# Performance work log

Measured on AMD Instinct MI355X. Metric: run time of the kernel, lower is better.

## Reference

```python
import jax, jax.numpy as jnp
import numpy as np

B, L_IN, D = 4, 4096, 1024
R_MIN, R_MAX = 0.9, 0.999


def setup_inputs() -> dict:
    key = jax.random.key(0)
    k0, k1, k2 = jax.random.split(key, 3)
    inputs = jax.random.normal(k0, (B, L_IN, D), jnp.float32)
    Wi = jax.random.normal(k1, (2 * D, D), jnp.float32) / np.sqrt(D)
    bi = jnp.zeros((2 * D,), jnp.float32)
    Wo = jax.random.normal(k2, (D, 2 * D), jnp.float32) / np.sqrt(2 * D)
    bo = jnp.zeros((D,), jnp.float32)
    # LRU stable-ring initialization, exactly as in the torch module
    rng = np.random.default_rng(0)
    u1 = rng.random(D)
    u2 = rng.random(D)
    v_log = np.log(-0.5 * np.log(u1 * (R_MAX ** 2 - R_MIN ** 2) + R_MIN ** 2))
    theta_log = np.log(u2 * np.pi * 2)
    gamma_log = np.log(np.sqrt(1.0 - np.exp(-np.exp(v_log)) ** 2))
    params_log = jnp.asarray(np.stack([v_log, theta_log, gamma_log]), jnp.float32)
    return {"inputs": inputs, "Wi": Wi, "bi": bi, "Wo": Wo, "bo": bo,
            "params_log": params_log}


def _lru_forward(inputs, Wi, bi, Wo, bo, params_log):
    b, l_in, d = inputs.shape
    u = inputs @ Wi.T + bi                      # [B, L, 2D]
    v, theta, gamma = jnp.exp(params_log)       # each [D]
    # torch.view_as_complex: interleaved (real, imag) pairs along last dim
    uc = u.reshape(b, l_in, d, 2)
    x = jax.lax.complex(uc[..., 0], uc[..., 1])  # [B, L, D] complex64
    log2_L = int(np.ceil(np.log2(l_in)))
    L = 2 ** log2_L
    x = jnp.pad(x, ((0, 0), (0, L - l_in), (0, 0)))
    # Blelloch-style log-depth scan: x_t = lambda * x_{t-1} + u_t,
    # lambda = exp(-v + i*theta)
    for i in range(1, log2_L + 1):
        blk = 2 ** i
        xb = x.reshape(b * L // blk, blk, d)
        x1, x2 = xb[:, : blk // 2], xb[:, blk // 2:]
        pos = jnp.arange(1, blk // 2 + 1, dtype=jnp.float32)  # [blk/2]
        lambs = jnp.exp(jax.lax.complex(-pos[:, None] * v,
                                        pos[:, None] * theta))  # [blk/2, D]
        x2 = x2 + lambs * x1[:, -1:]
        x = jnp.concatenate([x1, x2], axis=1).reshape(b, L, d)
    x = x[:, :l_in] * gamma.astype(x.dtype)     # normalize, drop padding
    xr = jnp.concatenate([x.real, x.imag], axis=-1)  # [B, L, 2D]
    out = xr @ Wo.T + bo
    return jax.nn.relu(out)


def reference(inputs, Wi, bi, Wo, bo, params_log):
    return _lru_forward(inputs, Wi, bi, Wo, bo, params_log)
```

## Files before the change

### kernel.cpp

```cpp
#include <hip/hip_runtime.h>

#define BB 4
#define LL 4096
#define DD 1024
#define SS 64
#define TT 64

typedef __attribute__((ext_vector_type(4))) float  floatx4;
typedef __attribute__((ext_vector_type(8))) short  shortx8;

static __device__ __forceinline__ unsigned short f2bf(float f) {
    unsigned int u = __float_as_uint(f);
    u += 0x7fffu + ((u >> 16) & 1u);
    return (unsigned short)(u >> 16);
}
static __device__ __forceinline__ float bf2f(unsigned short h) {
    return __uint_as_float(((unsigned int)h) << 16);
}

#define NIN4 (BB * LL * DD / 4)
#define NW4  (2 * DD * DD / 4)
__global__ void cast_all_kernel(const float4* __restrict__ s_in, ushort4* __restrict__ d_inb,
                                const float4* __restrict__ s_wi, ushort4* __restrict__ d_wib,
                                const float4* __restrict__ s_wo, ushort4* __restrict__ d_wob) {
    int i = blockIdx.x * blockDim.x + threadIdx.x;
    const float4* s; ushort4* d; int j;
    if (i < NIN4)                 { s = s_in; d = d_inb; j = i; }
    else if (i < NIN4 + NW4)      { s = s_wi; d = d_wib; j = i - NIN4; }
    else                          { s = s_wo; d = d_wob; j = i - NIN4 - NW4; }
    float4 v = s[j];
    ushort4 o;
    o.x = f2bf(v.x); o.y = f2bf(v.y); o.z = f2bf(v.z); o.w = f2bf(v.w);
    d[j] = o;
}

template<int K, int NT, int EPI>
__global__ __launch_bounds__(256)
void gemm_bt(const unsigned short* __restrict__ A,
             const unsigned short* __restrict__ B,
             const float* __restrict__ bias,
             void* __restrict__ Cp) {
    constexpr int N = NT * 128;
    __shared__ __align__(16) short As[128 * 64];
    __shared__ __align__(16) short Bs[128 * 64];

    const int tid = threadIdx.x;
    const int b   = blockIdx.x;
    const int xcd = b & 7;
    const int i2  = b >> 3;
    const int tileM = ((i2 / NT) * 8 + xcd) * 128;
    const int tileN = (i2 % NT) * 128;

    const int lane  = tid & 63;
    const int wave  = tid >> 6;
    const int wm    = (wave >> 1) * 64;
    const int wn    = (wave & 1) * 64;
    const int r16   = lane & 15;
    const int quad  = lane >> 4;

    floatx4 acc[4][4] = {};

    int rowS[4], colS[4];
#pragma unroll
    for (int n = 0; n < 4; ++n) {
        const int q = tid + n * 256;
        rowS[n] = q >> 3;
        colS[n] = ((q & 7) ^ (rowS[n] & 7)) * 8;
    }
    const int ldsBase = (tid & ~63) * 8;

    const int fx = r16 & 7;

    for (int k0 = 0; k0 < K; k0 += 64) {
#pragma unroll
        for (int n = 0; n < 4; ++n) {
            __builtin_amdgcn_global_load_lds(
                (const __attribute__((address_space(1))) void*)&A[(size_t)(tileM + rowS[n]) * K + k0 + colS[n]],
                (__attribute__((address_space(3))) void*)&As[ldsBase + n * 2048], 16, 0, 0);
            __builtin_amdgcn_global_load_lds(
                (const __attribute__((address_space(1))) void*)&B[(size_t)(tileN + rowS[n]) * K + k0 + colS[n]],
                (__attribute__((address_space(3))) void*)&Bs[ldsBase + n * 2048], 16, 0, 0);
        }
        __syncthreads();

#pragma unroll
        for (int kk = 0; kk < 2; ++kk) {
            const int slot = ((kk * 4 + quad) ^ fx) * 8;
            shortx8 af[4], bfv[4];
#pragma unroll
            for (int i = 0; i < 4; ++i)
                af[i] = *(const shortx8*)(&As[(wm + i * 16 + r16) * 64 + slot]);
#pragma unroll
            for (int j = 0; j < 4; ++j)
                bfv[j] = *(const shortx8*)(&Bs[(wn + j * 16 + r16) * 64 + slot]);
#pragma unroll
            for (int i = 0; i < 4; ++i)
#pragma unroll
                for (int j = 0; j < 4; ++j)
                    acc[i][j] = __builtin_amdgcn_mfma_f32_16x16x32_bf16(
                        af[i], bfv[j], acc[i][j], 0, 0, 0);
        }
        __syncthreads();
    }

#pragma unroll
    for (int i = 0; i < 4; ++i) {
#pragma unroll
        for (int j = 0; j < 4; ++j) {
            const int col = tileN + wn + j * 16 + r16;
            const float bv = bias[col];
#pragma unroll
            for (int r = 0; r < 4; ++r) {
                const int row = tileM + wm + i * 16 + quad * 4 + r;
                float v = acc[i][j][r] + bv;
                if (EPI == 0) {
                    ((unsigned short*)Cp)[(size_t)row * N + col] = f2bf(v);
                } else {
                    ((float*)Cp)[(size_t)row * N + col] = fmaxf(v, 0.0f);
                }
            }
        }
    }
}

__global__ __launch_bounds__(256)
void scanA(const unsigned short* __restrict__ u,
           const float* __restrict__ plog,
           float2* __restrict__ Eend) {
    const int d0 = (blockIdx.x * 256 + threadIdx.x) * 2;
    const int c = blockIdx.y, b = blockIdx.z;
    const float v0  = expf(plog[d0]),      v1  = expf(plog[d0 + 1]);
    const float th0 = expf(plog[DD + d0]), th1 = expf(plog[DD + d0 + 1]);
    const float a0 = expf(-v0), a1 = expf(-v1);
    const float lr0 = a0 * cosf(th0), li0 = a0 * sinf(th0);
    const float lr1 = a1 * cosf(th1), li1 = a1 * sinf(th1);
    float zr0 = 0.f, zi0 = 0.f, zr1 = 0.f, zi1 = 0.f;
    const unsigned short* up = u + (size_t)(b * LL + c * TT) * (2 * DD) + 2 * d0;
#pragma unroll 4
    for (int tl = 0; tl < TT; ++tl) {
        uint2 pr = *(const uint2*)up;
        float xr0 = bf2f((unsigned short)(pr.x & 0xffffu));
        float xi0 = bf2f((unsigned short)(pr.x >> 16));
        float xr1 = bf2f((unsigned short)(pr.y & 0xffffu));
        float xi1 = bf2f((unsigned short)(pr.y >> 16));
        float t;
        t = lr0 * zr0 - li0 * zi0 + xr0; zi0 = lr0 * zi0 + li0 * zr0 + xi0; zr0 = t;
        t = lr1 * zr1 - li1 * zi1 + xr1; zi1 = lr1 * zi1 + li1 * zr1 + xi1; zr1 = t;
        up += 2 * DD;
    }
    *(float4*)&Eend[(size_t)c * (BB * DD) + b * DD + d0] =
        make_float4(zr0, zi0, zr1, zi1);
}

__global__ __launch_bounds__(256)
void scanC(const unsigned short* __restrict__ u,
           const float* __restrict__ plog,
           const float2* __restrict__ Eend,
           unsigned short* __restrict__ xr) {
    const int d0 = (blockIdx.x * 256 + threadIdx.x) * 2;
    const int c = blockIdx.y, b = blockIdx.z;
    const float v0  = expf(plog[d0]),      v1  = expf(plog[d0 + 1]);
    const float th0 = expf(plog[DD + d0]), th1 = expf(plog[DD + d0 + 1]);
    const float g0  = expf(plog[2 * DD + d0]), g1 = expf(plog[2 * DD + d0 + 1]);
    const float a0 = expf(-v0), a1 = expf(-v1);
    const float lr0 = a0 * cosf(th0), li0 = a0 * sinf(th0);
    const float lr1 = a1 * cosf(th1), li1 = a1 * sinf(th1);

    const float aT0 = expf(-(float)TT * v0), aT1 = expf(-(float)TT * v1);
    const float Lr0 = aT0 * cosf((float)TT * th0), Li0 = aT0 * sinf((float)TT * th0);
    const float Lr1 = aT1 * cosf((float)TT * th1), Li1 = aT1 * sinf((float)TT * th1);
    float yr0 = 0.f, yi0 = 0.f, yr1 = 0.f, yi1 = 0.f;
    for (int cc = 0; cc < c; ++cc) {
        float4 e = *(const float4*)&Eend[(size_t)cc * (BB * DD) + b * DD + d0];
        float t;
        t = Lr0 * yr0 - Li0 * yi0 + e.x; yi0 = Lr0 * yi0 + Li0 * yr0 + e.y; yr0 = t;
        t = Lr1 * yr1 - Li1 * yi1 + e.z; yi1 = Lr1 * yi1 + Li1 * yr1 + e.w; yr1 = t;
    }

    const unsigned short* up = u + (size_t)(b * LL + c * TT) * (2 * DD) + 2 * d0;
    unsigned short* xp = xr + (size_t)(b * LL + c * TT) * (2 * DD) + d0;
#pragma unroll 4
    for (int tl = 0; tl < TT; ++tl) {
        uint2 pr = *(const uint2*)up;
        float xr0 = bf2f((unsigned short)(pr.x & 0xffffu));
        float xi0 = bf2f((unsigned short)(pr.x >> 16));
        float xr1 = bf2f((unsigned short)(pr.y & 0xffffu));
        float xi1 = bf2f((unsigned short)(pr.y >> 16));
        float t;
        t = lr0 * yr0 - li0 * yi0 + xr0; yi0 = lr0 * yi0 + li0 * yr0 + xi0; yr0 = t;
        t = lr1 * yr1 - li1 * yi1 + xr1; yi1 = lr1 * yi1 + li1 * yr1 + xi1; yr1 = t;
        *(unsigned int*)&xp[0]  = (unsigned int)f2bf(g0 * yr0) |
                                  ((unsigned int)f2bf(g1 * yr1) << 16);
        *(unsigned int*)&xp[DD] = (unsigned int)f2bf(g0 * yi0) |
                                  ((unsigned int)f2bf(g1 * yi1) << 16);
        up += 2 * DD;
        xp += 2 * DD;
    }
}

extern "C" void kernel_launch(void* const* d_in, const int* in_sizes, int n_in,
                              void* d_out, int out_size, void* d_ws, size_t ws_size,
                              hipStream_t stream) {
    const float* inputs = (const float*)d_in[0];
    const float* Wi     = (const float*)d_in[1];
    const float* bi     = (const float*)d_in[2];
    const float* Wo     = (const float*)d_in[3];
    const float* bo     = (const float*)d_in[4];
    const float* plog   = (const float*)d_in[5];
    float* out = (float*)d_out;

    const size_t M = (size_t)BB * LL;
    unsigned short* u_bf  = (unsigned short*)d_ws;
    unsigned short* xr_bf = u_bf  + M * 2 * DD;
    unsigned short* in_bf = xr_bf + M * 2 * DD;
    unsigned short* Wi_bf = in_bf + M * DD;
    unsigned short* Wo_bf = Wi_bf + (size_t)2 * DD * DD;
    float2* Eend = (float2*)(Wo_bf + (size_t)2 * DD * DD);

    {
        int total4 = NIN4 + 2 * NW4;
        cast_all_kernel<<<total4 / 256, 256, 0, stream>>>(
            (const float4*)inputs, (ushort4*)in_bf,
            (const float4*)Wi,     (ushort4*)Wi_bf,
            (const float4*)Wo,     (ushort4*)Wo_bf);
    }

    gemm_bt<DD, 16, 0><<<(M / 128) * 16, 256, 0, stream>>>(
        in_bf, Wi_bf, bi, (void*)u_bf);

    scanA<<<dim3(DD / 512, SS, BB), 256, 0, stream>>>(u_bf, plog, Eend);
    scanC<<<dim3(DD / 512, SS, BB), 256, 0, stream>>>(u_bf, plog, Eend, xr_bf);

    gemm_bt<2 * DD, 8, 1><<<(M / 128) * 8, 256, 0, stream>>>(
        xr_bf, Wo_bf, bo, (void*)out);
}
```

Baseline: 335.5 us.

## Replace GEMM with 256x256 tile, double-buffered, 8-wave pipelined kernel

Replaces the 128x128 single-buffer bf16 GEMM with a 256x256-tile kernel that uses 512 threads, double-buffered LDS and staged global-to-LDS loads. These loads are interleaved with quadrant-wise MFMA phases, with setprio around the MFMA bursts. The aim is to hide global load latency behind compute and raise arithmetic intensity per LDS byte. The cost is 128KB of LDS and many barriers per k-step, which limits occupancy. The hand-tuned vmcnt waits also carry a correctness risk.

```diff
diff --git a/kernel.cpp b/kernel.cpp
--- a/kernel.cpp
+++ b/kernel.cpp
@@ -35,92 +35,138 @@
 }
 
 template<int K, int NT, int EPI>
-__global__ __launch_bounds__(256)
-void gemm_bt(const unsigned short* __restrict__ A,
+__global__ __launch_bounds__(512, 2)
+void gemm256(const unsigned short* __restrict__ A,
              const unsigned short* __restrict__ B,
              const float* __restrict__ bias,
              void* __restrict__ Cp) {
-    constexpr int N = NT * 128;
-    __shared__ __align__(16) short As[128 * 64];
-    __shared__ __align__(16) short Bs[128 * 64];
+    constexpr int N   = NT * 256;
+    constexpr int NKT = K / 64;
+    __shared__ __align__(16) short As[2][256 * 64];
+    __shared__ __align__(16) short Bs[2][256 * 64];
 
     const int tid = threadIdx.x;
-    const int b   = blockIdx.x;
-    const int xcd = b & 7;
-    const int i2  = b >> 3;
-    const int tileM = ((i2 / NT) * 8 + xcd) * 128;
-    const int tileN = (i2 % NT) * 128;
-
-    const int lane  = tid & 63;
-    const int wave  = tid >> 6;
-    const int wm    = (wave >> 1) * 64;
-    const int wn    = (wave & 1) * 64;
-    const int r16   = lane & 15;
-    const int quad  = lane >> 4;
-
-    floatx4 acc[4][4] = {};
-
-    int rowS[4], colS[4];
+    const int blk = blockIdx.x;
+    const int xcd = blk & 7;
+    const int i2  = blk >> 3;
+    const int tileM = ((i2 / NT) * 8 + xcd) * 256;
+    const int tileN = (i2 % NT) * 256;
+
+    const int lane   = tid & 63;
+    const int wave   = tid >> 6;
+    const int wave_m = wave >> 2;
+    const int wave_n = wave & 3;
+    const int r16    = lane & 15;
+    const int quad   = lane >> 4;
+    const int slotx  = r16 & 7;
+    const int wmRow  = wave_m * 64 + r16;
+    const int wnRow  = wave_n * 32 + r16;
+
+    const int srow = tid >> 3;
+    const int scol = ((tid & 7) ^ (srow & 7)) * 8;
+    const int ldsChunkBase = (tid & ~63) * 8;
+    const size_t aOff = (size_t)(tileM + srow) * K + scol;
+    const size_t bOff = (size_t)(tileN + srow) * K + scol;
+
+    floatx4 acc[8][4] = {};
+    shortx8 af[4][2], bf0v[2][2], bf1v[2][2];
+
+#define GLL(SRC, DST) __builtin_amdgcn_global_load_lds( \
+        (const __attribute__((address_space(1))) void*)(SRC), \
+        (__attribute__((address_space(3))) void*)(DST), 16, 0, 0)
+#define STAGE_A(BUF, H, KT) do { \
+    GLL(A + aOff + (size_t)((H) * 128) * K + (KT) * 64,      &As[BUF][(H) * 8192 + ldsChunkBase]); \
+    GLL(A + aOff + (size_t)((H) * 128 + 64) * K + (KT) * 64, &As[BUF][(H) * 8192 + 4096 + ldsChunkBase]); \
+} while (0)
+#define STAGE_B(BUF, H, KT) do { \
+    GLL(B + bOff + (size_t)((H) * 128) * K + (KT) * 64,      &Bs[BUF][(H) * 8192 + ldsChunkBase]); \
+    GLL(B + bOff + (size_t)((H) * 128 + 64) * K + (KT) * 64, &Bs[BUF][(H) * 8192 + 4096 + ldsChunkBase]); \
+} while (0)
+#define LOAD_A(BUF, MH) do { \
+    _Pragma("unroll") for (int il = 0; il < 4; ++il) \
+    _Pragma("unroll") for (int kk = 0; kk < 2; ++kk) \
+        af[il][kk] = *(const shortx8*)&As[BUF][((MH) * 128 + wmRow + il * 16) * 64 + ((kk * 4 + quad) ^ slotx) * 8]; \
+} while (0)
+#define LOAD_B(BUF, NH, DST) do { \
+    _Pragma("unroll") for (int jl = 0; jl < 2; ++jl) \
+    _Pragma("unroll") for (int kk = 0; kk < 2; ++kk) \
+        DST[jl][kk] = *(const shortx8*)&Bs[BUF][((NH) * 128 + wnRow + jl * 16) * 64 + ((kk * 4 + quad) ^ slotx) * 8]; \
+} while (0)
+#define MFMAQ(MH, NH, BF) do { \
+    __builtin_amdgcn_s_setprio(1); \
+    _Pragma("unroll") for (int kk = 0; kk < 2; ++kk) \
+    _Pragma("unroll") for (int il = 0; il < 4; ++il) \
+    _Pragma("unroll") for (int jl = 0; jl < 2; ++jl) \
+        acc[(MH) * 4 + il][(NH) * 2 + jl] = __builtin_amdgcn_mfma_f32_16x16x32_bf16( \
+            af[il][kk], BF[jl][kk], acc[(MH) * 4 + il][(NH) * 2 + jl], 0, 0, 0); \
+    __builtin_amdgcn_s_setprio(0); \
+} while (0)
+
+    STAGE_A(0, 0, 0);
+    STAGE_B(0, 0, 0);
+    STAGE_B(0, 1, 0);
+    STAGE_A(0, 1, 0);
+    STAGE_A(1, 0, 1);
+    STAGE_B(1, 1, 1);
+    STAGE_A(1, 1, 1);
+    asm volatile("s_waitcnt vmcnt(6)" ::: "memory");
+    __builtin_amdgcn_s_barrier();
+
+    for (int t = 0; t < NKT; ++t) {
+        const int cb = t & 1;
+        const int t1 = (t + 1 < NKT) ? t + 1 : NKT - 1;
+        const int t2 = (t + 2 < NKT) ? t + 2 : NKT - 1;
+        LOAD_A(cb, 0);
+        LOAD_B(cb, 0, bf0v);
+        STAGE_B(cb ^ 1, 0, t1);
+        __builtin_amdgcn_s_barrier();
+        asm volatile("s_waitcnt lgkmcnt(0)" ::: "memory");
+        MFMAQ(0, 0, bf0v);
+        __builtin_amdgcn_s_barrier();
+        LOAD_B(cb, 1, bf1v);
+        STAGE_A(cb, 0, t2);
+        __builtin_amdgcn_s_barrier();
+        asm volatile("s_waitcnt lgkmcnt(0)" ::: "memory");
+        MFMAQ(0, 1, bf1v);
+        __builtin_amdgcn_s_barrier();
+        LOAD_A(cb, 1);
+        STAGE_B(cb, 1, t2);
+        __builtin_amdgcn_s_barrier();
+        asm volatile("s_waitcnt lgkmcnt(0)" ::: "memory");
+        MFMAQ(1, 0, bf0v);
+        __builtin_amdgcn_s_barrier();
+        STAGE_A(cb, 1, t2);
+        asm volatile("s_waitcnt vmcnt(6)" ::: "memory");
+        __builtin_amdgcn_s_barrier();
+        MFMAQ(1, 1, bf1v);
+        __builtin_amdgcn_s_barrier();
+    }
+    asm volatile("s_waitcnt vmcnt(0)" ::: "memory");
+
 #pragma unroll
-    for (int n = 0; n < 4; ++n) {
-        const int q = tid + n * 256;
-        rowS[n] = q >> 3;
-        colS[n] = ((q & 7) ^ (rowS[n] & 7)) * 8;
-    }
-    const int ldsBase = (tid & ~63) * 8;
-
-    const int fx = r16 & 7;
-
-    for (int k0 = 0; k0 < K; k0 += 64) {
-#pragma unroll
-        for (int n = 0; n < 4; ++n) {
-            __builtin_amdgcn_global_load_lds(
-                (const __attribute__((address_space(1))) void*)&A[(size_t)(tileM + rowS[n]) * K + k0 + colS[n]],
-                (__attribute__((address_space(3))) void*)&As[ldsBase + n * 2048], 16, 0, 0);
-            __builtin_amdgcn_global_load_lds(
-                (const __attribute__((address_space(1))) void*)&B[(size_t)(tileN + rowS[n]) * K + k0 + colS[n]],
-                (__attribute__((address_space(3))) void*)&Bs[ldsBase + n * 2048], 16, 0, 0);
-        }
-        __syncthreads();
-
-#pragma unroll
-        for (int kk = 0; kk < 2; ++kk) {
-            const int slot = ((kk * 4 + quad) ^ fx) * 8;
-            shortx8 af[4], bfv[4];
-#pragma unroll
-            for (int i = 0; i < 4; ++i)
-                af[i] = *(const shortx8*)(&As[(wm + i * 16 + r16) * 64 + slot]);
-#pragma unroll
-            for (int j = 0; j < 4; ++j)
-                bfv[j] = *(const shortx8*)(&Bs[(wn + j * 16 + r16) * 64 + slot]);
-#pragma unroll
-            for (int i = 0; i < 4; ++i)
-#pragma unroll
-                for (int j = 0; j < 4; ++j)
-                    acc[i][j] = __builtin_amdgcn_mfma_f32_16x16x32_bf16(
-                        af[i], bfv[j], acc[i][j], 0, 0, 0);
-        }
-        __syncthreads();
-    }
-
-#pragma unroll
-    for (int i = 0; i < 4; ++i) {
+    for (int i = 0; i < 8; ++i) {
+        const int row0 = tileM + (i >> 2) * 128 + wave_m * 64 + (i & 3) * 16 + quad * 4;
 #pragma unroll
         for (int j = 0; j < 4; ++j) {
-            const int col = tileN + wn + j * 16 + r16;
+            const int col = tileN + (j >> 1) * 128 + wave_n * 32 + (j & 1) * 16 + r16;
             const float bv = bias[col];
 #pragma unroll
             for (int r = 0; r < 4; ++r) {
-                const int row = tileM + wm + i * 16 + quad * 4 + r;
                 float v = acc[i][j][r] + bv;
                 if (EPI == 0) {
-                    ((unsigned short*)Cp)[(size_t)row * N + col] = f2bf(v);
+                    ((unsigned short*)Cp)[(size_t)(row0 + r) * N + col] = f2bf(v);
                 } else {
-                    ((float*)Cp)[(size_t)row * N + col] = fmaxf(v, 0.0f);
+                    ((float*)Cp)[(size_t)(row0 + r) * N + col] = fmaxf(v, 0.0f);
                 }
             }
         }
     }
+#undef GLL
+#undef STAGE_A
+#undef STAGE_B
+#undef LOAD_A
+#undef LOAD_B
+#undef MFMAQ
 }
 
 __global__ __launch_bounds__(256)
@@ -225,12 +271,12 @@
             (const float4*)Wo,     (ushort4*)Wo_bf);
     }
 
-    gemm_bt<DD, 16, 0><<<(M / 128) * 16, 256, 0, stream>>>(
+    gemm256<DD, 8, 0><<<(M / 256) * 8, 512, 0, stream>>>(
         in_bf, Wi_bf, bi, (void*)u_bf);
 
     scanA<<<dim3(DD / 512, SS, BB), 256, 0, stream>>>(u_bf, plog, Eend);
     scanC<<<dim3(DD / 512, SS, BB), 256, 0, stream>>>(u_bf, plog, Eend, xr_bf);
 
-    gemm_bt<2 * DD, 8, 1><<<(M / 128) * 8, 256, 0, stream>>>(
+    gemm256<2 * DD, 4, 1><<<(M / 256) * 4, 512, 0, stream>>>(
         xr_bf, Wo_bf, bo, (void*)out);
 }
```

Result: faster. 306.2 us (-8.7%).
